# Kernel optimization log

Measured on AMD Instinct MI355X. Metric: run time of the kernel, lower is better.

Reference implementation:

```python
import jax, jax.numpy as jnp
import numpy as np

EMBD = 384
FFN = 4 * EMBD
T = 200
NH = 6
HS = EMBD // NH
B = 256


def _layernorm(x, g, b, eps=1e-5):
    m = jnp.mean(x, axis=-1, keepdims=True)
    v = jnp.mean((x - m) ** 2, axis=-1, keepdims=True)
    return (x - m) * jax.lax.rsqrt(v + eps) * g + b


def setup_inputs() -> dict:
    key = jax.random.key(0)
    ks = jax.random.split(key, 10)
    s = EMBD ** -0.5
    return {
        "x": jax.random.normal(ks[0], (B, T, EMBD), dtype=jnp.float32),
        "Wq": jax.random.normal(ks[1], (EMBD, EMBD), dtype=jnp.float32) * s,
        "Wk": jax.random.normal(ks[2], (EMBD, EMBD), dtype=jnp.float32) * s,
        "Wv": jax.random.normal(ks[3], (EMBD, EMBD), dtype=jnp.float32) * s,
        "Wproj": jax.random.normal(ks[4], (EMBD, EMBD), dtype=jnp.float32) * s,
        "bproj": jnp.zeros((EMBD,), dtype=jnp.float32),
        "W1": jax.random.normal(ks[5], (EMBD, FFN), dtype=jnp.float32) * s,
        "b1": jnp.zeros((FFN,), dtype=jnp.float32),
        "W2": jax.random.normal(ks[6], (FFN, EMBD), dtype=jnp.float32) * (FFN ** -0.5),
        "b2": jnp.zeros((EMBD,), dtype=jnp.float32),
        "g1": jnp.ones((EMBD,), dtype=jnp.float32),
        "be1": jnp.zeros((EMBD,), dtype=jnp.float32),
        "g2": jnp.ones((EMBD,), dtype=jnp.float32),
        "be2": jnp.zeros((EMBD,), dtype=jnp.float32),
    }


def reference(x, Wq, Wk, Wv, Wproj, bproj, W1, b1, W2, b2, g1, be1, g2, be2):
    # pre-LN attention
    h = _layernorm(x, g1, be1)
    Bb, Tt, _ = h.shape
    q = (h @ Wq).reshape(Bb, Tt, NH, HS)
    k = (h @ Wk).reshape(Bb, Tt, NH, HS)
    v = (h @ Wv).reshape(Bb, Tt, NH, HS)
    # NOTE: original scales by C**-0.5 where C = embd (not head_size)
    scores = jnp.einsum("bthd,bshd->bhts", q, k) * (EMBD ** -0.5)
    causal = jnp.tril(jnp.ones((Tt, Tt), dtype=bool))
    scores = jnp.where(causal, scores, -jnp.inf)
    wei = jax.nn.softmax(scores, axis=-1)
    att = jnp.einsum("bhts,bshd->bthd", wei, v).reshape(Bb, Tt, EMBD)
    x = x + att @ Wproj + bproj
    # FFN (dropout is identity in eval mode)
    h2 = _layernorm(x, g2, be2)
    ffn = jax.nn.relu(h2 @ W1 + b1) @ W2 + b2
    return x + ffn
```

## Files before the change

kernel.cpp:

```cpp
#include <hip/hip_runtime.h>

#define EMBD 384
#define FFN_DIM 1536
#define T_SEQ 200
#define NHEAD 6
#define BATCH 256

typedef __bf16 bf16x8_t __attribute__((ext_vector_type(8)));
typedef short s16x8_t __attribute__((ext_vector_type(8)));
typedef float f32x4_t __attribute__((ext_vector_type(4)));

__device__ __forceinline__ float bf2f(unsigned short h) {
  return __builtin_bit_cast(float, (unsigned)h << 16);
}
__device__ __forceinline__ unsigned short f2bf(float f) {
  unsigned u = __builtin_bit_cast(unsigned, f);
  u += 0x7fffu + ((u >> 16) & 1u);
  return (unsigned short)(u >> 16);
}
__device__ __forceinline__ void async_cp16(const void* g, void* l) {
  __builtin_amdgcn_global_load_lds(
      (const __attribute__((address_space(1))) unsigned int*)g,
      (__attribute__((address_space(3))) unsigned int*)l, 16, 0, 0);
}

__global__ void detect_dtype(const unsigned short* __restrict__ xr, int* __restrict__ flag) {
  int tid = threadIdx.x;
  int cnt = 0;
  for (int i = tid; i < 4096; i += 256) {
    float a = fabsf(bf2f(xr[2 * i]));
    cnt += (a > 1e-5f && a < 32.f) ? 1 : 0;
  }
#pragma unroll
  for (int off = 32; off; off >>= 1) cnt += __shfl_xor(cnt, off);
  __shared__ int tot;
  if (tid == 0) tot = 0;
  __syncthreads();
  if ((tid & 63) == 0) atomicAdd(&tot, cnt);
  __syncthreads();
  if (tid == 0) *flag = (tot > 2048) ? 1 : 0;
}

__global__ void cvt_vec(const void* __restrict__ src, float* __restrict__ dst, int n,
                        const int* __restrict__ flagp) {
  int i = blockIdx.x * 256 + threadIdx.x;
  if (i >= n) return;
  dst[i] = (*flagp) ? bf2f(((const unsigned short*)src)[i]) : ((const float*)src)[i];
}

__global__ void pack_w(const void* __restrict__ W, unsigned short* __restrict__ Wt,
                       int K, int N, int ldt, const int* __restrict__ flagp) {
  int idx = blockIdx.x * 256 + threadIdx.x;
  if (idx >= K * N) return;
  int k = idx / N, n = idx % N;
  unsigned short v = (*flagp) ? ((const unsigned short*)W)[idx]
                              : f2bf(((const float*)W)[idx]);
  Wt[(size_t)n * ldt + k] = v;
}

__global__ __launch_bounds__(256) void ln_kernel(const void* __restrict__ xin, int row0,
                                                 const float* __restrict__ g,
                                                 const float* __restrict__ be,
                                                 unsigned short* __restrict__ out,
                                                 const int* __restrict__ flagp) {
  int rloc = blockIdx.x * 4 + (threadIdx.x >> 6);
  int lane = threadIdx.x & 63;
  int isbf = flagp ? *flagp : 0;
  size_t row = (size_t)(row0 + rloc);
  float v[6];
  float sum = 0.f;
  if (isbf) {
    const unsigned short* xr = (const unsigned short*)xin + row * EMBD;
#pragma unroll
    for (int i = 0; i < 6; ++i) { v[i] = bf2f(xr[lane + 64 * i]); sum += v[i]; }
  } else {
    const float* xr = (const float*)xin + row * EMBD;
#pragma unroll
    for (int i = 0; i < 6; ++i) { v[i] = xr[lane + 64 * i]; sum += v[i]; }
  }
#pragma unroll
  for (int off = 32; off; off >>= 1) sum += __shfl_xor(sum, off);
  float mean = sum * (1.f / EMBD);
  float var = 0.f;
#pragma unroll
  for (int i = 0; i < 6; ++i) { float d = v[i] - mean; var += d * d; }
#pragma unroll
  for (int off = 32; off; off >>= 1) var += __shfl_xor(var, off);
  float rstd = rsqrtf(var * (1.f / EMBD) + 1e-5f);
  unsigned short* orow = out + (size_t)rloc * EMBD;
#pragma unroll
  for (int i = 0; i < 6; ++i) {
    int c = lane + 64 * i;
    orow[c] = f2bf((v[i] - mean) * rstd * g[c] + be[c]);
  }
}

template <int MODE>
__global__ __launch_bounds__(256, 3) void gemm_kernel(
    const unsigned short* __restrict__ A, int lda,
    const unsigned short* __restrict__ Bt, int K,
    const float* __restrict__ bias,
    const void* __restrict__ R, int ldr, int rrow0,
    void* __restrict__ Cv, int ldc, int crow0,
    int Mrows, const int* __restrict__ flagp) {
  __shared__ unsigned short As[128 * 64];
  __shared__ unsigned short Bs[128 * 64];
  const int n0 = blockIdx.x * 128;
  const int m0 = blockIdx.y * 128;
  const int tid = threadIdx.x;
  const int wv = tid >> 6, lane = tid & 63;
  const int wr = wv >> 1, wc = wv & 1;
  const int l = lane & 15, quad = lane >> 4;
  f32x4_t acc[4][4];
#pragma unroll
  for (int i = 0; i < 4; ++i)
#pragma unroll
    for (int j = 0; j < 4; ++j) acc[i][j] = (f32x4_t){0.f, 0.f, 0.f, 0.f};

  for (int kc = 0; kc < K; kc += 64) {
#pragma unroll
    for (int i = 0; i < 4; ++i) {
      int c = (wv * 4 + i) * 64 + lane;
      int row = c >> 3;
      int kk = ((c & 7) ^ (row & 7)) * 8;
      int ar = m0 + row;
      if (ar >= Mrows) ar = Mrows - 1;
      async_cp16(A + (size_t)ar * lda + kc + kk, As + (wv * 4 + i) * 512);
    }
#pragma unroll
    for (int i = 0; i < 4; ++i) {
      int c = (wv * 4 + i) * 64 + lane;
      int row = c >> 3;
      int kk = ((c & 7) ^ (row & 7)) * 8;
      async_cp16(Bt + (size_t)(n0 + row) * K + kc + kk, Bs + (wv * 4 + i) * 512);
    }
    __syncthreads();
#pragma unroll
    for (int ks = 0; ks < 2; ++ks) {
      bf16x8_t af[4], bfr[4];
#pragma unroll
      for (int g = 0; g < 4; ++g) {
        int row = wr * 64 + g * 16 + l;
        int ch = row * 8 + ((quad + ks * 4) ^ (row & 7));
        af[g] = *(const bf16x8_t*)&As[ch * 8];
        int nrw = wc * 64 + g * 16 + l;
        int nch = nrw * 8 + ((quad + ks * 4) ^ (nrw & 7));
        bfr[g] = *(const bf16x8_t*)&Bs[nch * 8];
      }
#pragma unroll
      for (int i = 0; i < 4; ++i)
#pragma unroll
        for (int j = 0; j < 4; ++j)
          acc[i][j] = __builtin_amdgcn_mfma_f32_16x16x32_bf16(af[i], bfr[j], acc[i][j], 0, 0, 0);
    }
    __syncthreads();
  }

  int isbf = flagp ? *flagp : 0;
#pragma unroll
  for (int i = 0; i < 4; ++i) {
#pragma unroll
    for (int j = 0; j < 4; ++j) {
#pragma unroll
      for (int r = 0; r < 4; ++r) {
        int row = m0 + wr * 64 + i * 16 + quad * 4 + r;
        int col = n0 + wc * 64 + j * 16 + l;
        if (row >= Mrows) continue;
        float v = acc[i][j][r];
        if (MODE == 0) {
          ((unsigned short*)Cv)[(size_t)row * ldc + col] = f2bf(v);
        } else if (MODE == 1) {
          v += bias[col];
          ((unsigned short*)Cv)[(size_t)row * ldc + col] = f2bf(fmaxf(v, 0.f));
        } else if (MODE == 2) {
          size_t ridx = (size_t)(rrow0 + row) * ldr + col;
          float rv = isbf ? bf2f(((const unsigned short*)R)[ridx]) : ((const float*)R)[ridx];
          ((float*)Cv)[(size_t)row * ldc + col] = v + bias[col] + rv;
        } else {
          float rv = ((const float*)R)[(size_t)row * ldr + col];
          float o = v + bias[col] + rv;
          size_t cidx = (size_t)(crow0 + row) * ldc + col;
          if (isbf)
            ((unsigned short*)Cv)[cidx] = f2bf(o);
          else
            ((float*)Cv)[cidx] = o;
        }
      }
    }
  }
}

__global__ __launch_bounds__(256, 1) void attn_kernel(const unsigned short* __restrict__ qkv,
                                                      unsigned short* __restrict__ att) {
  __shared__ unsigned short Ks[208 * 64];
  __shared__ unsigned short Vt[64 * 232];
  __shared__ unsigned short Ps[64 * 232];
  const int bh = blockIdx.x;
  const int b = bh / NHEAD, h = bh % NHEAD;
  const size_t base = (size_t)b * T_SEQ * 1152;
  const int tid = threadIdx.x;
  const int w = tid >> 6, lane = tid & 63;
  const int l = lane & 15, quad = lane >> 4;

  for (int i = w; i < 26; i += 4) {
    int c = i * 64 + lane;
    int s = c >> 3;
    int kk = ((c & 7) ^ (s & 7)) * 8;
    async_cp16(qkv + base + (size_t)s * 1152 + 384 + h * 64 + kk, Ks + i * 512);
  }
  for (int idx = tid; idx < 1600; idx += 256) {
    int s = idx >> 3, d0 = (idx & 7) * 8;
    s16x8_t vv = *(const s16x8_t*)(qkv + base + (size_t)s * 1152 + 768 + h * 64 + d0);
#pragma unroll
    for (int i = 0; i < 8; ++i) Vt[(d0 + i) * 232 + s] = (unsigned short)vv[i];
  }
  for (int idx = tid; idx < 64 * 32; idx += 256) {
    int d = idx >> 5, c = idx & 31;
    Vt[d * 232 + 200 + c] = 0;
  }
  __syncthreads();

  const float scale = 0.051031036307982884f;
  for (int t0 = 0; t0 < T_SEQ; t0 += 64) {
    if (t0 + w * 16 >= T_SEQ) continue;
    int tq = t0 + w * 16 + l;
    const unsigned short* qp = qkv + base + (size_t)tq * 1152 + h * 64;
    bf16x8_t qa0 = *(const bf16x8_t*)(qp + quad * 8);
    bf16x8_t qa1 = *(const bf16x8_t*)(qp + 32 + quad * 8);
    const int cmax = (t0 >> 4) + w + 1;
    f32x4_t sa[13];
#pragma unroll
    for (int c = 0; c < 13; ++c) {
      if (c < cmax) {
        int s = c * 16 + l;
        int ch0 = s * 8 + (quad ^ (s & 7));
        int ch1 = s * 8 + ((quad + 4) ^ (s & 7));
        bf16x8_t kb0 = *(const bf16x8_t*)&Ks[ch0 * 8];
        bf16x8_t kb1 = *(const bf16x8_t*)&Ks[ch1 * 8];
        f32x4_t z = (f32x4_t){0.f, 0.f, 0.f, 0.f};
        z = __builtin_amdgcn_mfma_f32_16x16x32_bf16(qa0, kb0, z, 0, 0, 0);
        sa[c] = __builtin_amdgcn_mfma_f32_16x16x32_bf16(qa1, kb1, z, 0, 0, 0);
      }
    }
    {
      s16x8_t zz = {0, 0, 0, 0, 0, 0, 0, 0};
#pragma unroll
      for (int i = 0; i < 8; ++i) {
        int c = i * 64 + lane;
        if (c < 464) *(s16x8_t*)&Ps[w * 16 * 232 + c * 8] = zz;
      }
    }
#pragma unroll
    for (int r = 0; r < 4; ++r) {
      int t = t0 + w * 16 + quad * 4 + r;
      float tv[13];
      float mx = -1e30f;
#pragma unroll
      for (int c = 0; c < 13; ++c) {
        if (c < cmax) {
          int col = c * 16 + l;
          float v = sa[c][r] * scale;
          tv[c] = (col <= t) ? v : -1e30f;
          mx = fmaxf(mx, tv[c]);
        }
      }
#pragma unroll
      for (int off = 1; off < 16; off <<= 1) mx = fmaxf(mx, __shfl_xor(mx, off));
      float sum = 0.f;
#pragma unroll
      for (int c = 0; c < 13; ++c) {
        if (c < cmax) {
          float p = __expf(tv[c] - mx);
          tv[c] = p;
          sum += p;
        }
      }
#pragma unroll
      for (int off = 1; off < 16; off <<= 1) sum += __shfl_xor(sum, off);
      float inv = 1.f / sum;
#pragma unroll
      for (int c = 0; c < 13; ++c) {
        if (c < cmax)
          Ps[(w * 16 + quad * 4 + r) * 232 + c * 16 + l] = f2bf(tv[c] * inv);
      }
    }
    int smax = t0 + w * 16 + 16;
    if (smax > T_SEQ) smax = T_SEQ;
    const int ksteps = (smax + 31) >> 5;
    f32x4_t oa[4];
#pragma unroll
    for (int d = 0; d < 4; ++d) oa[d] = (f32x4_t){0.f, 0.f, 0.f, 0.f};
    for (int ks = 0; ks < ksteps; ++ks) {
      bf16x8_t pa = *(const bf16x8_t*)&Ps[(w * 16 + l) * 232 + ks * 32 + quad * 8];
#pragma unroll
      for (int d = 0; d < 4; ++d) {
        bf16x8_t vb = *(const bf16x8_t*)&Vt[(d * 16 + l) * 232 + ks * 32 + quad * 8];
        oa[d] = __builtin_amdgcn_mfma_f32_16x16x32_bf16(pa, vb, oa[d], 0, 0, 0);
      }
    }
#pragma unroll
    for (int d = 0; d < 4; ++d) {
#pragma unroll
      for (int r = 0; r < 4; ++r) {
        int t = t0 + w * 16 + quad * 4 + r;
        if (t < T_SEQ)
          att[((size_t)b * T_SEQ + t) * EMBD + h * 64 + d * 16 + l] = f2bf(oa[d][r]);
      }
    }
  }
}

static constexpr size_t OFF_WQKV  = 0;
static constexpr size_t OFF_WPROJ = OFF_WQKV  + (size_t)1152 * 384 * 2;
static constexpr size_t OFF_W1    = OFF_WPROJ + (size_t)384 * 384 * 2;
static constexpr size_t OFF_W2    = OFF_W1    + (size_t)1536 * 384 * 2;
static constexpr size_t OFF_BIAS  = OFF_W2    + (size_t)384 * 1536 * 2;
static constexpr size_t OFF_FLAG  = OFF_BIAS  + 4096 * 4;
static constexpr size_t OFF_DYN   = OFF_FLAG + 256;

extern "C" void kernel_launch(void* const* d_in, const int* in_sizes, int n_in,
                              void* d_out, int out_size, void* d_ws, size_t ws_size,
                              hipStream_t stream) {
  const void* x     = d_in[0];
  const void* Wq    = d_in[1];
  const void* Wk    = d_in[2];
  const void* Wv    = d_in[3];
  const void* Wproj = d_in[4];
  const void* bproj = d_in[5];
  const void* W1    = d_in[6];
  const void* b1    = d_in[7];
  const void* W2    = d_in[8];
  const void* b2    = d_in[9];
  const void* g1    = d_in[10];
  const void* be1   = d_in[11];
  const void* g2    = d_in[12];
  const void* be2   = d_in[13];

  char* ws = (char*)d_ws;
  unsigned short* wqkv_t  = (unsigned short*)(ws + OFF_WQKV);
  unsigned short* wproj_t = (unsigned short*)(ws + OFF_WPROJ);
  unsigned short* w1_t    = (unsigned short*)(ws + OFF_W1);
  unsigned short* w2_t    = (unsigned short*)(ws + OFF_W2);
  float*          bias_f  = (float*)(ws + OFF_BIAS);
  int*            flag    = (int*)(ws + OFF_FLAG);

  int Bc = BATCH;
  while (Bc > 1 && OFF_DYN + (size_t)Bc * T_SEQ * 6144 > ws_size) Bc >>= 1;
  if (OFF_DYN + (size_t)Bc * T_SEQ * 6144 > ws_size) return;
  const int NC = BATCH / Bc;
  const int Mc = Bc * T_SEQ;
  const int mtiles = (Mc + 127) / 128;

  char* bufA = ws + OFF_DYN;
  char* bufB = bufA + (size_t)Mc * 2304;
  char* bufC = bufB + (size_t)Mc * 768;
  unsigned short* qkv = (unsigned short*)bufA;
  float*          x2  = (float*)bufA;
  unsigned short* h2  = (unsigned short*)(bufA + (size_t)Mc * 1536);
  unsigned short* hb  = (unsigned short*)bufB;
  unsigned short* mid = (unsigned short*)bufC;

  detect_dtype<<<1, 256, 0, stream>>>((const unsigned short*)x, flag);
  cvt_vec<<<2, 256, 0, stream>>>(bproj, bias_f + 0,    384,  flag);
  cvt_vec<<<6, 256, 0, stream>>>(b1,    bias_f + 384,  1536, flag);
  cvt_vec<<<2, 256, 0, stream>>>(b2,    bias_f + 1920, 384,  flag);
  cvt_vec<<<2, 256, 0, stream>>>(g1,    bias_f + 2304, 384,  flag);
  cvt_vec<<<2, 256, 0, stream>>>(be1,   bias_f + 2688, 384,  flag);
  cvt_vec<<<2, 256, 0, stream>>>(g2,    bias_f + 3072, 384,  flag);
  cvt_vec<<<2, 256, 0, stream>>>(be2,   bias_f + 3456, 384,  flag);
  pack_w<<<576, 256, 0, stream>>>(Wq,    wqkv_t,                 384,  384,  384,  flag);
  pack_w<<<576, 256, 0, stream>>>(Wk,    wqkv_t + 384 * 384,     384,  384,  384,  flag);
  pack_w<<<576, 256, 0, stream>>>(Wv,    wqkv_t + 2 * 384 * 384, 384,  384,  384,  flag);
  pack_w<<<576, 256, 0, stream>>>(Wproj, wproj_t,                384,  384,  384,  flag);
  pack_w<<<2304, 256, 0, stream>>>(W1,   w1_t,                   384,  1536, 384,  flag);
  pack_w<<<2304, 256, 0, stream>>>(W2,   w2_t,                   1536, 384,  1536, flag);

  for (int c = 0; c < NC; ++c) {
    const int row0 = c * Bc * T_SEQ;
    ln_kernel<<<Mc / 4, 256, 0, stream>>>(x, row0, bias_f + 2304, bias_f + 2688, hb, flag);
    gemm_kernel<0><<<dim3(9, mtiles), 256, 0, stream>>>(
        hb, 384, wqkv_t, 384, nullptr, nullptr, 0, 0, qkv, 1152, 0, Mc, nullptr);
    attn_kernel<<<Bc * NHEAD, 256, 0, stream>>>(qkv, hb);
    gemm_kernel<2><<<dim3(3, mtiles), 256, 0, stream>>>(
        hb, 384, wproj_t, 384, bias_f + 0, x, 384, row0, x2, 384, 0, Mc, flag);
    ln_kernel<<<Mc / 4, 256, 0, stream>>>(x2, 0, bias_f + 3072, bias_f + 3456, h2, nullptr);
    gemm_kernel<1><<<dim3(12, mtiles), 256, 0, stream>>>(
        h2, 384, w1_t, 384, bias_f + 384, nullptr, 0, 0, mid, 1536, 0, Mc, nullptr);
    gemm_kernel<3><<<dim3(3, mtiles), 256, 0, stream>>>(
        mid, 1536, w2_t, 1536, bias_f + 1920, x2, 384, 0, d_out, 384, row0, Mc, flag);
  }
}
```

Measured before the change: 781.2 us.

## Merge setup kernels, XCD-aware GEMM tiling, bf16 residual, vectorized LN, attention tweaks

Merges the seven bias-conversion launches and six weight-pack launches into one launch each. Remaps the GEMM grid so row tiles are spread across XCDs. Stores the intermediate residual x2 in bf16 instead of fp32, which halves that traffic but lowers precision. Vectorizes layernorm to 8 elements per lane. In attention, K is read directly from global memory instead of being staged in LDS, which frees shared memory for two blocks per CU, and the P buffer is zeroed once instead of on every tile.

```diff
diff --git a/kernel.cpp b/kernel.cpp
--- a/kernel.cpp
+++ b/kernel.cpp
@@ -41,20 +41,53 @@
   if (tid == 0) *flag = (tot > 2048) ? 1 : 0;
 }
 
-__global__ void cvt_vec(const void* __restrict__ src, float* __restrict__ dst, int n,
-                        const int* __restrict__ flagp) {
+__global__ void cvt_all(const void* bproj, const void* b1, const void* b2,
+                        const void* g1, const void* be1, const void* g2, const void* be2,
+                        float* __restrict__ dst, const int* __restrict__ flagp) {
   int i = blockIdx.x * 256 + threadIdx.x;
-  if (i >= n) return;
-  dst[i] = (*flagp) ? bf2f(((const unsigned short*)src)[i]) : ((const float*)src)[i];
-}
-
-__global__ void pack_w(const void* __restrict__ W, unsigned short* __restrict__ Wt,
-                       int K, int N, int ldt, const int* __restrict__ flagp) {
+  if (i >= 3840) return;
+  const void* src; int loc;
+  if (i < 384)       { src = bproj; loc = i; }
+  else if (i < 1920) { src = b1;    loc = i - 384; }
+  else if (i < 2304) { src = b2;    loc = i - 1920; }
+  else if (i < 2688) { src = g1;    loc = i - 2304; }
+  else if (i < 3072) { src = be1;   loc = i - 2688; }
+  else if (i < 3456) { src = g2;    loc = i - 3072; }
+  else               { src = be2;   loc = i - 3456; }
+  dst[i] = (*flagp) ? bf2f(((const unsigned short*)src)[loc]) : ((const float*)src)[loc];
+}
+
+static constexpr size_t OFF_WQKV  = 0;
+static constexpr size_t OFF_WPROJ = OFF_WQKV  + (size_t)1152 * 384 * 2;
+static constexpr size_t OFF_W1    = OFF_WPROJ + (size_t)384 * 384 * 2;
+static constexpr size_t OFF_W2    = OFF_W1    + (size_t)1536 * 384 * 2;
+static constexpr size_t OFF_BIAS  = OFF_W2    + (size_t)384 * 1536 * 2;
+static constexpr size_t OFF_FLAG  = OFF_BIAS  + 4096 * 4;
+static constexpr size_t OFF_DYN   = OFF_FLAG + 256;
+
+__global__ void pack_all(const void* Wq, const void* Wk, const void* Wv, const void* Wp,
+                         const void* W1, const void* W2, char* __restrict__ ws,
+                         const int* __restrict__ flagp) {
   int idx = blockIdx.x * 256 + threadIdx.x;
-  if (idx >= K * N) return;
-  int k = idx / N, n = idx % N;
-  unsigned short v = (*flagp) ? ((const unsigned short*)W)[idx]
-                              : f2bf(((const float*)W)[idx]);
+  if (idx >= 1769472) return;
+  const void* W; unsigned short* Wt; int loc, K, N, ldt;
+  if (idx < 589824) {
+    int which = idx / 147456;
+    loc = idx - which * 147456; K = 384; N = 384; ldt = 384;
+    if (which == 0)      { W = Wq; Wt = (unsigned short*)(ws + OFF_WQKV); }
+    else if (which == 1) { W = Wk; Wt = (unsigned short*)(ws + OFF_WQKV) + 147456; }
+    else if (which == 2) { W = Wv; Wt = (unsigned short*)(ws + OFF_WQKV) + 294912; }
+    else                 { W = Wp; Wt = (unsigned short*)(ws + OFF_WPROJ); }
+  } else if (idx < 1179648) {
+    loc = idx - 589824; K = 384; N = 1536; ldt = 384;
+    W = W1; Wt = (unsigned short*)(ws + OFF_W1);
+  } else {
+    loc = idx - 1179648; K = 1536; N = 384; ldt = 1536;
+    W = W2; Wt = (unsigned short*)(ws + OFF_W2);
+  }
+  int k = loc / N, n = loc % N;
+  unsigned short v = (*flagp) ? ((const unsigned short*)W)[loc]
+                              : f2bf(((const float*)W)[loc]);
   Wt[(size_t)n * ldt + k] = v;
 }
 
@@ -62,36 +95,46 @@
                                                  const float* __restrict__ g,
                                                  const float* __restrict__ be,
                                                  unsigned short* __restrict__ out,
-                                                 const int* __restrict__ flagp) {
+                                                 int isbf_mode, const int* __restrict__ flagp) {
   int rloc = blockIdx.x * 4 + (threadIdx.x >> 6);
   int lane = threadIdx.x & 63;
-  int isbf = flagp ? *flagp : 0;
+  int isbf = (isbf_mode >= 0) ? isbf_mode : *flagp;
   size_t row = (size_t)(row0 + rloc);
-  float v[6];
+  float v[8];
   float sum = 0.f;
-  if (isbf) {
-    const unsigned short* xr = (const unsigned short*)xin + row * EMBD;
-#pragma unroll
-    for (int i = 0; i < 6; ++i) { v[i] = bf2f(xr[lane + 64 * i]); sum += v[i]; }
+  const int act = lane < 48;
+  const int c0 = lane * 8;
+  if (act) {
+    if (isbf) {
+      s16x8_t xv = *(const s16x8_t*)((const unsigned short*)xin + row * EMBD + c0);
+#pragma unroll
+      for (int i = 0; i < 8; ++i) { v[i] = bf2f((unsigned short)xv[i]); sum += v[i]; }
+    } else {
+      const float* xr = (const float*)xin + row * EMBD + c0;
+#pragma unroll
+      for (int i = 0; i < 8; ++i) { v[i] = xr[i]; sum += v[i]; }
+    }
   } else {
-    const float* xr = (const float*)xin + row * EMBD;
-#pragma unroll
-    for (int i = 0; i < 6; ++i) { v[i] = xr[lane + 64 * i]; sum += v[i]; }
+#pragma unroll
+    for (int i = 0; i < 8; ++i) v[i] = 0.f;
   }
 #pragma unroll
   for (int off = 32; off; off >>= 1) sum += __shfl_xor(sum, off);
   float mean = sum * (1.f / EMBD);
   float var = 0.f;
-#pragma unroll
-  for (int i = 0; i < 6; ++i) { float d = v[i] - mean; var += d * d; }
+  if (act) {
+#pragma unroll
+    for (int i = 0; i < 8; ++i) { float d = v[i] - mean; var += d * d; }
+  }
 #pragma unroll
   for (int off = 32; off; off >>= 1) var += __shfl_xor(var, off);
   float rstd = rsqrtf(var * (1.f / EMBD) + 1e-5f);
-  unsigned short* orow = out + (size_t)rloc * EMBD;
-#pragma unroll
-  for (int i = 0; i < 6; ++i) {
-    int c = lane + 64 * i;
-    orow[c] = f2bf((v[i] - mean) * rstd * g[c] + be[c]);
+  if (act) {
+    s16x8_t ov;
+#pragma unroll
+    for (int i = 0; i < 8; ++i)
+      ov[i] = (short)f2bf((v[i] - mean) * rstd * g[c0 + i] + be[c0 + i]);
+    *(s16x8_t*)(out + (size_t)rloc * EMBD + c0) = ov;
   }
 }
 
@@ -102,11 +145,16 @@
     const float* __restrict__ bias,
     const void* __restrict__ R, int ldr, int rrow0,
     void* __restrict__ Cv, int ldc, int crow0,
-    int Mrows, const int* __restrict__ flagp) {
+    int Mrows, int NX, int NY, const int* __restrict__ flagp) {
   __shared__ unsigned short As[128 * 64];
   __shared__ unsigned short Bs[128 * 64];
-  const int n0 = blockIdx.x * 128;
-  const int m0 = blockIdx.y * 128;
+  const int g = blockIdx.x;
+  const int xcd = g & 7, s = g >> 3;
+  const int j = s / NX, xn = s - j * NX;
+  const int y = xcd + 8 * j;
+  if (y >= NY) return;
+  const int n0 = xn * 128;
+  const int m0 = y * 128;
   const int tid = threadIdx.x;
   const int wv = tid >> 6, lane = tid & 63;
   const int wr = wv >> 1, wc = wv & 1;
@@ -115,7 +163,7 @@
 #pragma unroll
   for (int i = 0; i < 4; ++i)
 #pragma unroll
-    for (int j = 0; j < 4; ++j) acc[i][j] = (f32x4_t){0.f, 0.f, 0.f, 0.f};
+    for (int jj = 0; jj < 4; ++jj) acc[i][jj] = (f32x4_t){0.f, 0.f, 0.f, 0.f};
 
   for (int kc = 0; kc < K; kc += 64) {
 #pragma unroll
@@ -139,34 +187,34 @@
     for (int ks = 0; ks < 2; ++ks) {
       bf16x8_t af[4], bfr[4];
 #pragma unroll
-      for (int g = 0; g < 4; ++g) {
-        int row = wr * 64 + g * 16 + l;
+      for (int gg = 0; gg < 4; ++gg) {
+        int row = wr * 64 + gg * 16 + l;
         int ch = row * 8 + ((quad + ks * 4) ^ (row & 7));
-        af[g] = *(const bf16x8_t*)&As[ch * 8];
-        int nrw = wc * 64 + g * 16 + l;
+        af[gg] = *(const bf16x8_t*)&As[ch * 8];
+        int nrw = wc * 64 + gg * 16 + l;
         int nch = nrw * 8 + ((quad + ks * 4) ^ (nrw & 7));
-        bfr[g] = *(const bf16x8_t*)&Bs[nch * 8];
+        bfr[gg] = *(const bf16x8_t*)&Bs[nch * 8];
       }
 #pragma unroll
       for (int i = 0; i < 4; ++i)
 #pragma unroll
-        for (int j = 0; j < 4; ++j)
-          acc[i][j] = __builtin_amdgcn_mfma_f32_16x16x32_bf16(af[i], bfr[j], acc[i][j], 0, 0, 0);
+        for (int jj = 0; jj < 4; ++jj)
+          acc[i][jj] = __builtin_amdgcn_mfma_f32_16x16x32_bf16(af[i], bfr[jj], acc[i][jj], 0, 0, 0);
     }
     __syncthreads();
   }
 
-  int isbf = flagp ? *flagp : 0;
+  int isbf = flagp ? *flagp : 1;
 #pragma unroll
   for (int i = 0; i < 4; ++i) {
 #pragma unroll
-    for (int j = 0; j < 4; ++j) {
+    for (int jj = 0; jj < 4; ++jj) {
 #pragma unroll
       for (int r = 0; r < 4; ++r) {
         int row = m0 + wr * 64 + i * 16 + quad * 4 + r;
-        int col = n0 + wc * 64 + j * 16 + l;
+        int col = n0 + wc * 64 + jj * 16 + l;
         if (row >= Mrows) continue;
-        float v = acc[i][j][r];
+        float v = acc[i][jj][r];
         if (MODE == 0) {
           ((unsigned short*)Cv)[(size_t)row * ldc + col] = f2bf(v);
         } else if (MODE == 1) {
@@ -175,9 +223,9 @@
         } else if (MODE == 2) {
           size_t ridx = (size_t)(rrow0 + row) * ldr + col;
           float rv = isbf ? bf2f(((const unsigned short*)R)[ridx]) : ((const float*)R)[ridx];
-          ((float*)Cv)[(size_t)row * ldc + col] = v + bias[col] + rv;
+          ((unsigned short*)Cv)[(size_t)row * ldc + col] = f2bf(v + bias[col] + rv);
         } else {
-          float rv = ((const float*)R)[(size_t)row * ldr + col];
+          float rv = bf2f(((const unsigned short*)R)[(size_t)row * ldr + col]);
           float o = v + bias[col] + rv;
           size_t cidx = (size_t)(crow0 + row) * ldc + col;
           if (isbf)
@@ -190,9 +238,8 @@
   }
 }
 
-__global__ __launch_bounds__(256, 1) void attn_kernel(const unsigned short* __restrict__ qkv,
+__global__ __launch_bounds__(256, 2) void attn_kernel(const unsigned short* __restrict__ qkv,
                                                       unsigned short* __restrict__ att) {
-  __shared__ unsigned short Ks[208 * 64];
   __shared__ unsigned short Vt[64 * 232];
   __shared__ unsigned short Ps[64 * 232];
   const int bh = blockIdx.x;
@@ -202,12 +249,6 @@
   const int w = tid >> 6, lane = tid & 63;
   const int l = lane & 15, quad = lane >> 4;
 
-  for (int i = w; i < 26; i += 4) {
-    int c = i * 64 + lane;
-    int s = c >> 3;
-    int kk = ((c & 7) ^ (s & 7)) * 8;
-    async_cp16(qkv + base + (size_t)s * 1152 + 384 + h * 64 + kk, Ks + i * 512);
-  }
   for (int idx = tid; idx < 1600; idx += 256) {
     int s = idx >> 3, d0 = (idx & 7) * 8;
     s16x8_t vv = *(const s16x8_t*)(qkv + base + (size_t)s * 1152 + 768 + h * 64 + d0);
@@ -218,9 +259,14 @@
     int d = idx >> 5, c = idx & 31;
     Vt[d * 232 + 200 + c] = 0;
   }
+  {
+    s16x8_t zz = {0, 0, 0, 0, 0, 0, 0, 0};
+    for (int idx = tid; idx < 1856; idx += 256) *(s16x8_t*)&Ps[idx * 8] = zz;
+  }
   __syncthreads();
 
   const float scale = 0.051031036307982884f;
+  const unsigned short* kp = qkv + base + 384 + h * 64;
   for (int t0 = 0; t0 < T_SEQ; t0 += 64) {
     if (t0 + w * 16 >= T_SEQ) continue;
     int tq = t0 + w * 16 + l;
@@ -232,22 +278,12 @@
 #pragma unroll
     for (int c = 0; c < 13; ++c) {
       if (c < cmax) {
-        int s = c * 16 + l;
-        int ch0 = s * 8 + (quad ^ (s & 7));
-        int ch1 = s * 8 + ((quad + 4) ^ (s & 7));
-        bf16x8_t kb0 = *(const bf16x8_t*)&Ks[ch0 * 8];
-        bf16x8_t kb1 = *(const bf16x8_t*)&Ks[ch1 * 8];
+        const unsigned short* kr = kp + (size_t)(c * 16 + l) * 1152;
+        bf16x8_t kb0 = *(const bf16x8_t*)(kr + quad * 8);
+        bf16x8_t kb1 = *(const bf16x8_t*)(kr + 32 + quad * 8);
         f32x4_t z = (f32x4_t){0.f, 0.f, 0.f, 0.f};
         z = __builtin_amdgcn_mfma_f32_16x16x32_bf16(qa0, kb0, z, 0, 0, 0);
         sa[c] = __builtin_amdgcn_mfma_f32_16x16x32_bf16(qa1, kb1, z, 0, 0, 0);
-      }
-    }
-    {
-      s16x8_t zz = {0, 0, 0, 0, 0, 0, 0, 0};
-#pragma unroll
-      for (int i = 0; i < 8; ++i) {
-        int c = i * 64 + lane;
-        if (c < 464) *(s16x8_t*)&Ps[w * 16 * 232 + c * 8] = zz;
       }
     }
 #pragma unroll
@@ -309,14 +345,6 @@
     }
   }
 }
-
-static constexpr size_t OFF_WQKV  = 0;
-static constexpr size_t OFF_WPROJ = OFF_WQKV  + (size_t)1152 * 384 * 2;
-static constexpr size_t OFF_W1    = OFF_WPROJ + (size_t)384 * 384 * 2;
-static constexpr size_t OFF_W2    = OFF_W1    + (size_t)1536 * 384 * 2;
-static constexpr size_t OFF_BIAS  = OFF_W2    + (size_t)384 * 1536 * 2;
-static constexpr size_t OFF_FLAG  = OFF_BIAS  + 4096 * 4;
-static constexpr size_t OFF_DYN   = OFF_FLAG + 256;
 
 extern "C" void kernel_launch(void* const* d_in, const int* in_sizes, int n_in,
                               void* d_out, int out_size, void* d_ws, size_t ws_size,
@@ -349,44 +377,34 @@
   if (OFF_DYN + (size_t)Bc * T_SEQ * 6144 > ws_size) return;
   const int NC = BATCH / Bc;
   const int Mc = Bc * T_SEQ;
-  const int mtiles = (Mc + 127) / 128;
+  const int NY = (Mc + 127) / 128;
+  const int NYpad = (NY + 7) & ~7;
 
   char* bufA = ws + OFF_DYN;
   char* bufB = bufA + (size_t)Mc * 2304;
   char* bufC = bufB + (size_t)Mc * 768;
   unsigned short* qkv = (unsigned short*)bufA;
-  float*          x2  = (float*)bufA;
-  unsigned short* h2  = (unsigned short*)(bufA + (size_t)Mc * 1536);
+  unsigned short* x2  = (unsigned short*)bufA;
+  unsigned short* h2  = (unsigned short*)(bufA + (size_t)Mc * 768);
   unsigned short* hb  = (unsigned short*)bufB;
   unsigned short* mid = (unsigned short*)bufC;
 
   detect_dtype<<<1, 256, 0, stream>>>((const unsigned short*)x, flag);
-  cvt_vec<<<2, 256, 0, stream>>>(bproj, bias_f + 0,    384,  flag);
-  cvt_vec<<<6, 256, 0, stream>>>(b1,    bias_f + 384,  1536, flag);
-  cvt_vec<<<2, 256, 0, stream>>>(b2,    bias_f + 1920, 384,  flag);
-  cvt_vec<<<2, 256, 0, stream>>>(g1,    bias_f + 2304, 384,  flag);
-  cvt_vec<<<2, 256, 0, stream>>>(be1,   bias_f + 2688, 384,  flag);
-  cvt_vec<<<2, 256, 0, stream>>>(g2,    bias_f + 3072, 384,  flag);
-  cvt_vec<<<2, 256, 0, stream>>>(be2,   bias_f + 3456, 384,  flag);
-  pack_w<<<576, 256, 0, stream>>>(Wq,    wqkv_t,                 384,  384,  384,  flag);
-  pack_w<<<576, 256, 0, stream>>>(Wk,    wqkv_t + 384 * 384,     384,  384,  384,  flag);
-  pack_w<<<576, 256, 0, stream>>>(Wv,    wqkv_t + 2 * 384 * 384, 384,  384,  384,  flag);
-  pack_w<<<576, 256, 0, stream>>>(Wproj, wproj_t,                384,  384,  384,  flag);
-  pack_w<<<2304, 256, 0, stream>>>(W1,   w1_t,                   384,  1536, 384,  flag);
-  pack_w<<<2304, 256, 0, stream>>>(W2,   w2_t,                   1536, 384,  1536, flag);
+  cvt_all<<<15, 256, 0, stream>>>(bproj, b1, b2, g1, be1, g2, be2, bias_f, flag);
+  pack_all<<<6912, 256, 0, stream>>>(Wq, Wk, Wv, Wproj, W1, W2, ws, flag);
 
   for (int c = 0; c < NC; ++c) {
     const int row0 = c * Bc * T_SEQ;
-    ln_kernel<<<Mc / 4, 256, 0, stream>>>(x, row0, bias_f + 2304, bias_f + 2688, hb, flag);
-    gemm_kernel<0><<<dim3(9, mtiles), 256, 0, stream>>>(
-        hb, 384, wqkv_t, 384, nullptr, nullptr, 0, 0, qkv, 1152, 0, Mc, nullptr);
+    ln_kernel<<<Mc / 4, 256, 0, stream>>>(x, row0, bias_f + 2304, bias_f + 2688, hb, -1, flag);
+    gemm_kernel<0><<<9 * NYpad, 256, 0, stream>>>(
+        hb, 384, wqkv_t, 384, nullptr, nullptr, 0, 0, qkv, 1152, 0, Mc, 9, NY, nullptr);
     attn_kernel<<<Bc * NHEAD, 256, 0, stream>>>(qkv, hb);
-    gemm_kernel<2><<<dim3(3, mtiles), 256, 0, stream>>>(
-        hb, 384, wproj_t, 384, bias_f + 0, x, 384, row0, x2, 384, 0, Mc, flag);
-    ln_kernel<<<Mc / 4, 256, 0, stream>>>(x2, 0, bias_f + 3072, bias_f + 3456, h2, nullptr);
-    gemm_kernel<1><<<dim3(12, mtiles), 256, 0, stream>>>(
-        h2, 384, w1_t, 384, bias_f + 384, nullptr, 0, 0, mid, 1536, 0, Mc, nullptr);
-    gemm_kernel<3><<<dim3(3, mtiles), 256, 0, stream>>>(
-        mid, 1536, w2_t, 1536, bias_f + 1920, x2, 384, 0, d_out, 384, row0, Mc, flag);
-  }
-}
+    gemm_kernel<2><<<3 * NYpad, 256, 0, stream>>>(
+        hb, 384, wproj_t, 384, bias_f + 0, x, 384, row0, x2, 384, 0, Mc, 3, NY, flag);
+    ln_kernel<<<Mc / 4, 256, 0, stream>>>(x2, 0, bias_f + 3072, bias_f + 3456, h2, 1, nullptr);
+    gemm_kernel<1><<<12 * NYpad, 256, 0, stream>>>(
+        h2, 384, w1_t, 384, bias_f + 384, nullptr, 0, 0, mid, 1536, 0, Mc, 12, NY, nullptr);
+    gemm_kernel<3><<<3 * NYpad, 256, 0, stream>>>(
+        mid, 1536, w2_t, 1536, bias_f + 1920, x2, 384, 0, d_out, 384, row0, Mc, 3, NY, flag);
+  }
+}
```

New measurement: 679.3 us. 1.15x faster.
